# Kernel tuning notes

Hardware: AMD Instinct MI355X
Metric: run time of the kernel (lower is better)

## Reference

```python
import jax, jax.numpy as jnp
import numpy as np

B, L, C, P_LEN = 512, 336, 321, 96
WIN, HID = 12, 25
PRED_SEG = P_LEN // WIN


def setup_inputs() -> dict:
    key = jax.random.key(0)
    ks = jax.random.split(key, 8)
    s = 1.0 / np.sqrt(HID)
    u = lambda k, shape: jax.random.uniform(k, shape, minval=-s, maxval=s, dtype=jnp.float32)
    return {
        "x": jax.random.normal(ks[0], (B, L, C), dtype=jnp.float32),
        "segmentor": jax.random.uniform(ks[1], (C, WIN, 1), dtype=jnp.float32),  # torch.rand init
        "W_ih": u(ks[2], (C, 4 * HID, 1)),
        "W_hh": u(ks[3], (C, 4 * HID, HID)),
        "b_ih": u(ks[4], (C, 4 * HID)),
        "b_hh": u(ks[5], (C, 4 * HID)),
        "Wp": u(ks[6], (C, 1, HID)),
        "bp": u(ks[7], (C, 1)),
        "pred_seg": PRED_SEG,
    }


def reference(x, segmentor, W_ih, W_hh, b_ih, b_hh, Wp, bp, pred_seg):
    b_, l_, c_ = x.shape
    w_ = segmentor.shape[1]
    s_ = l_ // w_
    h_ = W_hh.shape[-1]

    seq_mean = jnp.mean(x, axis=1, keepdims=True)            # [B,1,C]
    xc = jnp.transpose(x - seq_mean, (0, 2, 1))              # [B,C,L]
    seg2d = segmentor[..., 0]                                # [C,W]
    # segment embedding: [B,C,S,W] @ [C,W] -> time-major [S,B,C]
    seg_in = jnp.einsum('bcsw,cw->sbc', xc.reshape(b_, c_, s_, w_), seg2d)

    Wx = W_ih[:, :, 0]                                       # [C,4H]
    bias = b_ih + b_hh                                       # [C,4H]

    def cell(h, c, xt):  # xt [B,C]; h,c [B,C,H]; torch gate order i,f,g,o
        gates = xt[..., None] * Wx[None] + jnp.einsum('bch,cgh->bcg', h, W_hh) + bias[None]
        i, f, g, o = jnp.split(gates, 4, axis=-1)
        c_new = jax.nn.sigmoid(f) * c + jax.nn.sigmoid(i) * jnp.tanh(g)
        h_new = jax.nn.sigmoid(o) * jnp.tanh(c_new)
        return h_new, c_new

    h0 = jnp.zeros((b_, c_, h_), x.dtype)
    c0 = jnp.zeros_like(h0)

    def enc(carry, xt):
        h, c = carry
        h, c = cell(h, c, xt)
        return (h, c), None

    (h, c), _ = jax.lax.scan(enc, (h0, c0), seg_in)

    def proj(h):  # [B,C,H] -> [B,C]
        return jnp.einsum('bch,ch->bc', h, Wp[:, 0, :]) + bp[:, 0][None]

    out0 = proj(h)

    def dec(carry, _):
        h, c, inp = carry
        h, c = cell(h, c, inp)
        out = proj(h)
        return (h, c, out), out

    _, rest = jax.lax.scan(dec, (h, c, out0), None, length=pred_seg - 1)
    preds = jnp.concatenate([out0[None], rest], axis=0)      # [P,B,C]
    preds = jnp.transpose(preds, (1, 2, 0))                  # [B,C,P]
    # de-segment: [B,C,P] x [C,W] -> [B,C,P*W]
    y = jnp.einsum('bcp,cw->bcpw', preds, seg2d).reshape(b_, c_, pred_seg * w_)
    return jnp.transpose(y, (0, 2, 1)) + seq_mean
```

## Files before the change

kernel.cpp:

```cpp
#include <hip/hip_runtime.h>
#include <math.h>

#define NB 512
#define NL 336
#define NC 321
#define NS 28
#define NW 12
#define NH 25
#define NP 8
#define NG 100
#define NT (NS + NP - 1)
#define BSL 16
#define WPB 4
#define NCHK 4
#define LOG2E 1.44269504088896340736f
#define N2LOG2E -2.88539008177792681472f

typedef __attribute__((ext_vector_type(8))) _Float16 f16x8;
typedef __attribute__((ext_vector_type(4))) float f32x4;

union F8 { f16x8 v; _Float16 h[8]; };

__device__ __forceinline__ void set_q3f(F8& b, bool q3, float xt) {
    b.h[1] = q3 ? (_Float16)xt : b.h[1];
    b.h[2] = q3 ? (_Float16)1.0f : b.h[2];
    b.h[3] = q3 ? (_Float16)0.0f : b.h[3];
    b.h[4] = q3 ? (_Float16)0.0f : b.h[4];
    b.h[5] = q3 ? (_Float16)0.0f : b.h[5];
    b.h[6] = q3 ? (_Float16)0.0f : b.h[6];
    b.h[7] = q3 ? (_Float16)0.0f : b.h[7];
}

extern "C" __global__ __launch_bounds__(384)
void k_seg_part(const float* __restrict__ x, const float* __restrict__ seg,
                float* __restrict__ seg_raw, float* __restrict__ psum) {
    const int b = blockIdx.x;
    const int ch = blockIdx.y;
    const int c = threadIdx.x;
    if (c >= NC) return;
    float sw[NW];
#pragma unroll
    for (int w = 0; w < NW; ++w) sw[w] = seg[c * NW + w];
    float acc[7];
    float s0 = 0.0f, s1 = 0.0f, s2 = 0.0f, s3 = 0.0f;
    const float* xb = x + ((size_t)b * NL + ch * 84) * NC + c;
#pragma unroll
    for (int i = 0; i < 7; ++i) {
        float a = 0.0f;
        float t0 = 0.0f, t1 = 0.0f, t2 = 0.0f, t3 = 0.0f;
#pragma unroll
        for (int w = 0; w < NW; w += 4) {
            const float v0 = xb[(i * NW + w) * NC];
            const float v1 = xb[(i * NW + w + 1) * NC];
            const float v2 = xb[(i * NW + w + 2) * NC];
            const float v3 = xb[(i * NW + w + 3) * NC];
            t0 += v0; t1 += v1; t2 += v2; t3 += v3;
            a = fmaf(v0, sw[w], a);
            a = fmaf(v1, sw[w + 1], a);
            a = fmaf(v2, sw[w + 2], a);
            a = fmaf(v3, sw[w + 3], a);
        }
        s0 += t0; s1 += t1; s2 += t2; s3 += t3;
        acc[i] = a;
    }
    psum[((size_t)ch * NB + b) * NC + c] = (s0 + s1) + (s2 + s3);
#pragma unroll
    for (int i = 0; i < 7; ++i) {
        const int s = ch * 7 + i;
        seg_raw[((size_t)s * NC + c) * NB + b] = acc[i];
    }
}

extern "C" __global__ __launch_bounds__(384)
void k_mean(const float* __restrict__ psum, float* __restrict__ meanw,
            float* __restrict__ meanT) {
    const int b = blockIdx.x;
    const int c = threadIdx.x;
    if (c >= NC) return;
    float s = 0.0f;
#pragma unroll
    for (int ch = 0; ch < NCHK; ++ch)
        s += psum[((size_t)ch * NB + b) * NC + c];
    const float mean = s * (1.0f / (float)NL);
    meanw[b * NC + c] = mean;
    meanT[(size_t)c * NB + b] = mean;
}

extern "C" __global__ __launch_bounds__(256, 4)
void k_lstm(const float* __restrict__ seg_raw, const float* __restrict__ W_ih,
            const float* __restrict__ W_hh, const float* __restrict__ b_ih,
            const float* __restrict__ b_hh, const float* __restrict__ Wp,
            const float* __restrict__ bp, const float* __restrict__ seg,
            const float* __restrict__ meanT, float* __restrict__ preds) {
    const int c = blockIdx.x;
    const int wv = threadIdx.x >> 6;
    const int lane = threadIdx.x & 63;
    const int b0 = (blockIdx.y * WPB + wv) * BSL;
    const int bb = lane & 15;
    const int q  = lane >> 4;
    const bool q3 = (q == 3);

    float ssc = 0.0f;
#pragma unroll
    for (int w = 0; w < NW; ++w) ssc += seg[c * NW + w];
    const float mml = meanT[(size_t)c * NB + b0 + bb];
    const float mcorr = mml * ssc;

    const int qq = bb >> 2, rr = bb & 3;
    const float srow = (rr == 2) ? 2.88539008177792681472f : LOG2E;
    const float* __restrict__ whh = W_hh + (size_t)c * NG * NH;
    const float* __restrict__ wxp = W_ih + (size_t)c * NG;
    const float* __restrict__ bip = b_ih + (size_t)c * NG;
    const float* __restrict__ bhp = b_hh + (size_t)c * NG;
    F8 afr[8];
#pragma unroll 1
    for (int mg = 0; mg < 8; ++mg) {
        const int jj = qq * 8 + mg;
        const int grow = rr * NH + jj;
        F8 f0;
#pragma unroll
        for (int e = 0; e < 8; ++e) {
            const int k = q * 8 + e;
            float v0 = 0.0f;
            if (jj < NH) {
                if (k < NH)         v0 = whh[grow * NH + k] * srow;
                else if (k == 25)   v0 = wxp[grow] * srow;
                else if (k == 26)   v0 = (bip[grow] + bhp[grow]) * srow;
            }
            f0.h[e] = (_Float16)v0;
        }
        afr[mg] = f0;
    }

    float wpl[8];
#pragma unroll
    for (int mg = 0; mg < 8; ++mg) {
        const int j = q * 8 + mg;
        wpl[mg] = (j < NH) ? Wp[(size_t)c * NH + j] : 0.0f;
    }
    const float bpc = bp[c];

    F8 ph;
    {
        const float x0 = seg_raw[(size_t)c * NB + b0 + bb] - mcorr;
#pragma unroll
        for (int e = 0; e < 8; ++e) ph.h[e] = (_Float16)0.0f;
        set_q3f(ph, q3, x0);
    }

    float cst[8];
#pragma unroll
    for (int mg = 0; mg < 8; ++mg) cst[mg] = 0.0f;

#pragma unroll 1
    for (int t = 0; t < NT; ++t) {
        const bool enc_next = (t + 1 < NS);
        const bool do_proj = (t >= NS - 1);
        const bool have_next = (t + 1 < NT);

        float xn = 0.0f;
        if (enc_next)
            xn = seg_raw[((size_t)(t + 1) * NC + c) * NB + b0 + bb] - mcorr;

        f32x4 av[8];
#pragma unroll
        for (int mg = 0; mg < 8; ++mg) {
            f32x4 z = {0.0f, 0.0f, 0.0f, 0.0f};
            av[mg] = __builtin_amdgcn_mfma_f32_16x16x32_f16(afr[mg].v, ph.v, z, 0, 0, 0);
        }

        float ei[8], ef[8], eg[8], eo[8];
#pragma unroll
        for (int mg = 0; mg < 8; ++mg) {
            ei[mg] = __builtin_amdgcn_exp2f(-av[mg][0]);
            ef[mg] = __builtin_amdgcn_exp2f(-av[mg][1]);
            eg[mg] = __builtin_amdgcn_exp2f(-av[mg][2]);
            eo[mg] = __builtin_amdgcn_exp2f(-av[mg][3]);
        }

        float hnv[8];
        float pp = 0.0f;
#pragma unroll
        for (int mg = 0; mg < 8; ++mg) {
            const float p1f = 1.0f + ef[mg];
            const float pig = (1.0f + ei[mg]) * (1.0f + eg[mg]);
            const float num = fmaf(cst[mg], pig, (1.0f - eg[mg]) * p1f);
            const float cn  = num * __builtin_amdgcn_rcpf(p1f * pig);
            const float et  = __builtin_amdgcn_exp2f(cn * N2LOG2E);
            const float hn  = (1.0f - et) *
                              __builtin_amdgcn_rcpf((1.0f + eo[mg]) * (1.0f + et));
            cst[mg] = cn;
            hnv[mg] = hn;
            if (do_proj) pp = fmaf(hn, wpl[mg], pp);
        }

        float ov = 0.0f;
        if (do_proj) {
            pp += __shfl_xor(pp, 16);
            pp += __shfl_xor(pp, 32);
            ov = pp + bpc;
            if (q == 0)
                preds[((size_t)c * NP + (t - (NS - 1))) * NB + b0 + bb] = ov;
        }

        if (have_next) {
#pragma unroll
            for (int e = 0; e < 8; ++e) ph.h[e] = (_Float16)hnv[e];
            set_q3f(ph, q3, enc_next ? xn : ov);
        }
    }
}

extern "C" __global__ __launch_bounds__(384)
void k_out(const float* __restrict__ preds, const float* __restrict__ seg,
           const float* __restrict__ meanw, float* __restrict__ out) {
    const int b = blockIdx.x;
    const int p = blockIdx.y;
    const int c = threadIdx.x;
    if (c >= NC) return;
    const float pv = preds[((size_t)c * NP + p) * NB + b];
    const float mean = meanw[b * NC + c];
    float* ob = out + ((size_t)b * (NP * NW) + p * NW) * NC + c;
#pragma unroll
    for (int w = 0; w < NW; ++w)
        ob[w * NC] = fmaf(pv, seg[c * NW + w], mean);
}

extern "C" void kernel_launch(void* const* d_in, const int* in_sizes, int n_in,
                              void* d_out, int out_size, void* d_ws, size_t ws_size,
                              hipStream_t stream) {
    const float* x    = (const float*)d_in[0];
    const float* seg  = (const float*)d_in[1];
    const float* W_ih = (const float*)d_in[2];
    const float* W_hh = (const float*)d_in[3];
    const float* b_ih = (const float*)d_in[4];
    const float* b_hh = (const float*)d_in[5];
    const float* Wp   = (const float*)d_in[6];
    const float* bp   = (const float*)d_in[7];
    float* out = (float*)d_out;

    float* seg_raw = (float*)d_ws;
    float* psum    = seg_raw + (size_t)NS * NC * NB;
    float* meanw   = psum + (size_t)NCHK * NB * NC;
    float* meanT   = meanw + (size_t)NB * NC;
    float* preds   = meanT + (size_t)NC * NB;

    k_seg_part<<<dim3(NB, NCHK), 384, 0, stream>>>(x, seg, seg_raw, psum);
    k_mean<<<NB, 384, 0, stream>>>(psum, meanw, meanT);
    k_lstm<<<dim3(NC, NB / (BSL * WPB)), 256, 0, stream>>>(
        seg_raw, W_ih, W_hh, b_ih, b_hh, Wp, bp, seg, meanT, preds);
    k_out<<<dim3(NB, NP), 384, 0, stream>>>(preds, seg, meanw, out);
}
```

Baseline: 337.5 us.

## Process two independent 16-batch slices per wavefront in LSTM kernel

Each wavefront now carries two independent 16-column batch slices through the recurrence, issuing two MFMAs per gate group and interleaving two independent gate/activation chains. This gives the scheduler independent work to hide MFMA and transcendental latency along the serial time loop, and halves the grid's y dimension so the A-fragment setup is amortized over twice the batch. It costs more VGPRs per thread, which could reduce occupancy under the 256x4 launch bound, and leaves fewer blocks to fill the device.

```diff
diff --git a/kernel.cpp b/kernel.cpp
--- a/kernel.cpp
+++ b/kernel.cpp
@@ -10,7 +10,7 @@
 #define NP 8
 #define NG 100
 #define NT (NS + NP - 1)
-#define BSL 16
+#define BSL 32
 #define WPB 4
 #define NCHK 4
 #define LOG2E 1.44269504088896340736f
@@ -103,8 +103,8 @@
     float ssc = 0.0f;
 #pragma unroll
     for (int w = 0; w < NW; ++w) ssc += seg[c * NW + w];
-    const float mml = meanT[(size_t)c * NB + b0 + bb];
-    const float mcorr = mml * ssc;
+    const float mc0 = meanT[(size_t)c * NB + b0 + bb] * ssc;
+    const float mc1 = meanT[(size_t)c * NB + b0 + 16 + bb] * ssc;
 
     const int qq = bb >> 2, rr = bb & 3;
     const float srow = (rr == 2) ? 2.88539008177792681472f : LOG2E;
@@ -140,17 +140,19 @@
     }
     const float bpc = bp[c];
 
-    F8 ph;
+    F8 ph0, ph1;
     {
-        const float x0 = seg_raw[(size_t)c * NB + b0 + bb] - mcorr;
-#pragma unroll
-        for (int e = 0; e < 8; ++e) ph.h[e] = (_Float16)0.0f;
-        set_q3f(ph, q3, x0);
-    }
-
-    float cst[8];
-#pragma unroll
-    for (int mg = 0; mg < 8; ++mg) cst[mg] = 0.0f;
+        const float x0 = seg_raw[(size_t)c * NB + b0 + bb] - mc0;
+        const float x1 = seg_raw[(size_t)c * NB + b0 + 16 + bb] - mc1;
+#pragma unroll
+        for (int e = 0; e < 8; ++e) { ph0.h[e] = (_Float16)0.0f; ph1.h[e] = (_Float16)0.0f; }
+        set_q3f(ph0, q3, x0);
+        set_q3f(ph1, q3, x1);
+    }
+
+    float cst0[8], cst1[8];
+#pragma unroll
+    for (int mg = 0; mg < 8; ++mg) { cst0[mg] = 0.0f; cst1[mg] = 0.0f; }
 
 #pragma unroll 1
     for (int t = 0; t < NT; ++t) {
@@ -158,55 +160,82 @@
         const bool do_proj = (t >= NS - 1);
         const bool have_next = (t + 1 < NT);
 
-        float xn = 0.0f;
-        if (enc_next)
-            xn = seg_raw[((size_t)(t + 1) * NC + c) * NB + b0 + bb] - mcorr;
-
-        f32x4 av[8];
+        float xn0 = 0.0f, xn1 = 0.0f;
+        if (enc_next) {
+            const float* p = seg_raw + ((size_t)(t + 1) * NC + c) * NB + b0;
+            xn0 = p[bb] - mc0;
+            xn1 = p[16 + bb] - mc1;
+        }
+
+        f32x4 av0[8], av1[8];
 #pragma unroll
         for (int mg = 0; mg < 8; ++mg) {
             f32x4 z = {0.0f, 0.0f, 0.0f, 0.0f};
-            av[mg] = __builtin_amdgcn_mfma_f32_16x16x32_f16(afr[mg].v, ph.v, z, 0, 0, 0);
-        }
-
-        float ei[8], ef[8], eg[8], eo[8];
+            av0[mg] = __builtin_amdgcn_mfma_f32_16x16x32_f16(afr[mg].v, ph0.v, z, 0, 0, 0);
+            av1[mg] = __builtin_amdgcn_mfma_f32_16x16x32_f16(afr[mg].v, ph1.v, z, 0, 0, 0);
+        }
+
+        float hnv0[8], hnv1[8];
+        float pp0 = 0.0f, pp1 = 0.0f;
 #pragma unroll
         for (int mg = 0; mg < 8; ++mg) {
-            ei[mg] = __builtin_amdgcn_exp2f(-av[mg][0]);
-            ef[mg] = __builtin_amdgcn_exp2f(-av[mg][1]);
-            eg[mg] = __builtin_amdgcn_exp2f(-av[mg][2]);
-            eo[mg] = __builtin_amdgcn_exp2f(-av[mg][3]);
-        }
-
-        float hnv[8];
-        float pp = 0.0f;
-#pragma unroll
-        for (int mg = 0; mg < 8; ++mg) {
-            const float p1f = 1.0f + ef[mg];
-            const float pig = (1.0f + ei[mg]) * (1.0f + eg[mg]);
-            const float num = fmaf(cst[mg], pig, (1.0f - eg[mg]) * p1f);
-            const float cn  = num * __builtin_amdgcn_rcpf(p1f * pig);
-            const float et  = __builtin_amdgcn_exp2f(cn * N2LOG2E);
-            const float hn  = (1.0f - et) *
-                              __builtin_amdgcn_rcpf((1.0f + eo[mg]) * (1.0f + et));
-            cst[mg] = cn;
-            hnv[mg] = hn;
-            if (do_proj) pp = fmaf(hn, wpl[mg], pp);
-        }
-
-        float ov = 0.0f;
+            {
+                const float ei = __builtin_amdgcn_exp2f(-av0[mg][0]);
+                const float ef = __builtin_amdgcn_exp2f(-av0[mg][1]);
+                const float eg = __builtin_amdgcn_exp2f(-av0[mg][2]);
+                const float eo = __builtin_amdgcn_exp2f(-av0[mg][3]);
+                const float p1f = 1.0f + ef;
+                const float pig = (1.0f + ei) * (1.0f + eg);
+                const float num = fmaf(cst0[mg], pig, (1.0f - eg) * p1f);
+                const float cn  = num * __builtin_amdgcn_rcpf(p1f * pig);
+                const float et  = __builtin_amdgcn_exp2f(cn * N2LOG2E);
+                const float hn  = (1.0f - et) *
+                                  __builtin_amdgcn_rcpf((1.0f + eo) * (1.0f + et));
+                cst0[mg] = cn;
+                hnv0[mg] = hn;
+                if (do_proj) pp0 = fmaf(hn, wpl[mg], pp0);
+            }
+            {
+                const float ei = __builtin_amdgcn_exp2f(-av1[mg][0]);
+                const float ef = __builtin_amdgcn_exp2f(-av1[mg][1]);
+                const float eg = __builtin_amdgcn_exp2f(-av1[mg][2]);
+                const float eo = __builtin_amdgcn_exp2f(-av1[mg][3]);
+                const float p1f = 1.0f + ef;
+                const float pig = (1.0f + ei) * (1.0f + eg);
+                const float num = fmaf(cst1[mg], pig, (1.0f - eg) * p1f);
+                const float cn  = num * __builtin_amdgcn_rcpf(p1f * pig);
+                const float et  = __builtin_amdgcn_exp2f(cn * N2LOG2E);
+                const float hn  = (1.0f - et) *
+                                  __builtin_amdgcn_rcpf((1.0f + eo) * (1.0f + et));
+                cst1[mg] = cn;
+                hnv1[mg] = hn;
+                if (do_proj) pp1 = fmaf(hn, wpl[mg], pp1);
+            }
+        }
+
+        float ov0 = 0.0f, ov1 = 0.0f;
         if (do_proj) {
-            pp += __shfl_xor(pp, 16);
-            pp += __shfl_xor(pp, 32);
-            ov = pp + bpc;
-            if (q == 0)
-                preds[((size_t)c * NP + (t - (NS - 1))) * NB + b0 + bb] = ov;
+            pp0 += __shfl_xor(pp0, 16);
+            pp0 += __shfl_xor(pp0, 32);
+            pp1 += __shfl_xor(pp1, 16);
+            pp1 += __shfl_xor(pp1, 32);
+            ov0 = pp0 + bpc;
+            ov1 = pp1 + bpc;
+            if (q == 0) {
+                float* pd = preds + ((size_t)c * NP + (t - (NS - 1))) * NB + b0;
+                pd[bb] = ov0;
+                pd[16 + bb] = ov1;
+            }
         }
 
         if (have_next) {
 #pragma unroll
-            for (int e = 0; e < 8; ++e) ph.h[e] = (_Float16)hnv[e];
-            set_q3f(ph, q3, enc_next ? xn : ov);
+            for (int e = 0; e < 8; ++e) {
+                ph0.h[e] = (_Float16)hnv0[e];
+                ph1.h[e] = (_Float16)hnv1[e];
+            }
+            set_q3f(ph0, q3, enc_next ? xn0 : ov0);
+            set_q3f(ph1, q3, enc_next ? xn1 : ov1);
         }
     }
 }
```

Measured after the change: 345.2 us. 1.02x slower.
